# Kernel optimization log

Measured on AMD Instinct MI355X. Metric: run time of the kernel, lower is better.

The kernel has to match this reference:

```python
import jax, jax.numpy as jnp
import numpy as np
from jax import lax

B, L, DDYN, DSTAT, H = 512, 64, 16, 8, 512
N_BANK, C_CAND, K_TOP, N_PROTO = 50000, 1024, 16, 8
T_TARG, Q_QUANT = 2, 3
TEMP = 0.2


def _l2norm(x, eps=1e-12):
    # matches torch.nn.functional.normalize: x / max(||x||, eps)
    n = jnp.sqrt(jnp.sum(x * x, axis=-1, keepdims=True))
    return x / jnp.maximum(n, eps)


def setup_inputs() -> dict:
    key = jax.random.key(0)
    ks = jax.random.split(key, 24)
    s = 0.02
    inp = {
        'sequence_values': jax.random.normal(ks[0], (B, L, DDYN), jnp.float32),
        'sequence_masks': jnp.ones((B, L), jnp.float32),
        'static_values': jax.random.normal(ks[1], (B, DSTAT), jnp.float32),
        'bank_keys': jax.random.normal(ks[2], (N_BANK, H), jnp.float32),
        'bank_values': jax.random.normal(ks[3], (N_BANK, H), jnp.float32),
        'candidate_indices': jax.random.randint(ks[4], (B, C_CAND), 0, N_BANK, jnp.int64),
        # encoder params (SequenceEncoder stand-in: masked-mean + linear + relu)
        'W_seq': jax.random.normal(ks[5], (DDYN, H), jnp.float32) * s,
        'W_stat': jax.random.normal(ks[6], (DSTAT, H), jnp.float32) * s,
        'b_enc': jnp.zeros((H,), jnp.float32),
        # retrieval / prototype / fusion params
        'W_q': jax.random.normal(ks[7], (H, H), jnp.float32) * s,
        'b_q': jnp.zeros((H,), jnp.float32),
        'prototype_tokens': jax.random.normal(ks[8], (N_PROTO, H), jnp.float32) * 0.02,
        'W_tr': jax.random.normal(ks[9], (2 * H, H), jnp.float32) * s,
        'b_tr': jnp.zeros((H,), jnp.float32),
        'W_gate': jax.random.normal(ks[10], (3 * H, H), jnp.float32) * s,
        'b_gate': jnp.zeros((H,), jnp.float32),
        'W_out': jax.random.normal(ks[11], (H, H), jnp.float32) * s,
        'b_out': jnp.zeros((H,), jnp.float32),
        # per-target heads stacked: [T, H, Q] and [T, H]
        'W_quant': jax.random.normal(ks[12], (T_TARG, H, Q_QUANT), jnp.float32) * s,
        'b_quant': jnp.zeros((T_TARG, Q_QUANT), jnp.float32),
        'W_ev': jax.random.normal(ks[13], (T_TARG, H), jnp.float32) * s,
        'b_ev': jnp.zeros((T_TARG,), jnp.float32),
    }
    return inp


def reference(sequence_values, sequence_masks, static_values, bank_keys, bank_values,
              candidate_indices, W_seq, W_stat, b_enc, W_q, b_q, prototype_tokens,
              W_tr, b_tr, W_gate, b_gate, W_out, b_out, W_quant, b_quant, W_ev, b_ev):
    # --- encoder (masked mean pool + linear + relu stand-in for SequenceEncoder) ---
    m = sequence_masks[..., None]                                   # [B,L,1]
    pooled = (sequence_values * m).sum(1) / jnp.maximum(m.sum(1), 1e-6)
    local_hidden = jax.nn.relu(pooled @ W_seq + static_values @ W_stat + b_enc)  # [B,H]

    # --- normalized query ---
    query = _l2norm(local_hidden @ W_q + b_q)                       # [B,H]

    # --- donor retrieval: gather + dot + topk + softmax + weighted sum ---
    cand_keys = bank_keys[candidate_indices]                        # [B,C,H]
    sim = jnp.einsum('bch,bh->bc', cand_keys, query)                # [B,C]
    top_scores, top_pos = lax.top_k(sim, K_TOP)                     # [B,K]
    weights = jax.nn.softmax(top_scores / max(TEMP, 1e-6), axis=-1)
    sel_idx = jnp.take_along_axis(candidate_indices, top_pos, axis=1)  # [B,K]
    donor_hidden = jnp.einsum('bk,bkh->bh', weights, bank_values[sel_idx])

    # --- prototype attention ---
    protos_n = _l2norm(prototype_tokens)                            # [P,H]
    pw = jax.nn.softmax(query @ protos_n.T, axis=-1)                # [B,P]
    proto_hidden = pw @ prototype_tokens                            # [B,H]

    # --- transfer / gate / fuse (dropout is identity at eval) ---
    transfer = jax.nn.relu(jnp.concatenate([donor_hidden, proto_hidden], -1) @ W_tr + b_tr)
    gate = jax.nn.sigmoid(
        jnp.concatenate([local_hidden, donor_hidden, proto_hidden], -1) @ W_gate + b_gate)
    fused = gate * local_hidden + (1.0 - gate) * transfer
    fused = jax.nn.relu(fused @ W_out + b_out)                      # [B,H]

    # --- heads: sorted quantiles [B,T,Q] and event logits [B,T] ---
    quant = jnp.sort(jnp.einsum('bh,thq->btq', fused, W_quant) + b_quant, axis=-1)
    logit = jnp.einsum('bh,th->bt', fused, W_ev) + b_ev
    return jnp.concatenate([quant.reshape(quant.shape[0], -1), logit], axis=-1)  # [B, T*Q+T]
```

## Files before the change

kernel.cpp:

```cpp
#include <hip/hip_runtime.h>
#include <hip/hip_bf16.h>

typedef __hip_bfloat16 bf16;
typedef float f4v __attribute__((ext_vector_type(4)));
typedef float f2v __attribute__((ext_vector_type(2)));

__device__ __forceinline__ float lo16(unsigned u){ return __uint_as_float(u << 16); }
__device__ __forceinline__ float hi16(unsigned u){ return __uint_as_float(u & 0xffff0000u); }

#define Bn 512
#define Hn 512
#define Cn 1024
#define Kn 16
#define NBANK 50000
#define NIDPAD 50176

__device__ __forceinline__ int clamp_id(int id){
    return (id < 0) ? 0 : ((id >= NBANK) ? (NBANK - 1) : id);
}

#define A_OFF    0
#define B_OFF    262144
#define C_OFF    524288
#define D_OFF    786432
#define SIM_OFF  1048576
#define ELO_OFF  1048576
#define EHI_OFF  1310720
#define F_OFF    1572864
#define G_OFF2   1835008
#define WS_FLOATS 2097152

#define HIST_I   0
#define CURSOR_I NIDPAD
#define GTOT_I   (2*NIDPAD)
#define OFFS_I   (2*NIDPAD + 256)

__global__ __launch_bounds__(256) void k_enc(
    const float* __restrict__ seq, const float* __restrict__ mask, const float* __restrict__ stat,
    const float* __restrict__ W_seq, const float* __restrict__ W_stat, const float* __restrict__ b_enc,
    const int* __restrict__ cand32, float* __restrict__ ws)
{
    const int b = blockIdx.x, t = threadIdx.x;
    const int h0 = 2*t, h1 = 2*t + 1;

    {
        const int c64 = ((cand32[1] | cand32[3] | cand32[5] | cand32[7]) == 0) ? 1 : 0;
        int* hist = (int*)(ws + F_OFF) + HIST_I;
        #pragma unroll
        for (int u = 0; u < 4; u++) {
            int idx = b*Cn + u*256 + t;
            atomicAdd(&hist[clamp_id(cand32[(size_t)idx << c64])], 1);
        }
    }

    __shared__ float s_pool[16], s_stat[8];
    if (t < 16) {
        float acc = 0.f, ms = 0.f;
        for (int l = 0; l < 64; l++) {
            float m = mask[b*64 + l];
            ms  += m;
            acc += seq[(b*64 + l)*16 + t] * m;
        }
        s_pool[t] = acc / fmaxf(ms, 1e-6f);
    } else if (t < 24) {
        s_stat[t - 16] = stat[b*8 + (t - 16)];
    }
    __syncthreads();
    float a0 = b_enc[h0], a1 = b_enc[h1];
    #pragma unroll
    for (int j = 0; j < 16; j++) {
        float2 wv = *(const float2*)(W_seq + j*Hn + h0);
        a0 += s_pool[j]*wv.x; a1 += s_pool[j]*wv.y;
    }
    #pragma unroll
    for (int j = 0; j < 8; j++) {
        float2 wv = *(const float2*)(W_stat + j*Hn + h0);
        a0 += s_stat[j]*wv.x; a1 += s_stat[j]*wv.y;
    }
    float* g = ws + B_OFF + (size_t)b*Hn;
    g[h0] = fmaxf(a0, 0.f); g[h1] = fmaxf(a1, 0.f);
}

__global__ __launch_bounds__(256) void k_scan(
    const int* __restrict__ hist, int* __restrict__ offs, int* __restrict__ gtot)
{
    __shared__ int s[256]; __shared__ int sbase;
    const int t = threadIdx.x, g = blockIdx.x*256 + t;
    const int v = hist[g];
    s[t] = v; __syncthreads();
    #pragma unroll
    for (int off = 1; off < 256; off <<= 1) {
        int x = (t >= off) ? s[t - off] : 0;
        __syncthreads();
        s[t] += x;
        __syncthreads();
    }
    if (t == 255) sbase = atomicAdd(gtot, s[255]);
    __syncthreads();
    offs[g] = sbase + s[t] - v;
}

__global__ __launch_bounds__(256) void k_scatter(
    const int* __restrict__ cand32, int* __restrict__ cursor,
    const int* __restrict__ offs, unsigned* __restrict__ refs)
{
    const int i = blockIdx.x*256 + threadIdx.x;
    const int c64 = ((cand32[1] | cand32[3] | cand32[5] | cand32[7]) == 0) ? 1 : 0;
    const int id = clamp_id(cand32[(size_t)i << c64]);
    const int pos = atomicAdd(&cursor[id], 1);
    refs[offs[id] + pos] = (unsigned)i;
}

__global__ __launch_bounds__(256) void k_qgemm_p(
    const float* __restrict__ W, const float* __restrict__ bias,
    const float* __restrict__ in,
    float* __restrict__ P0, float* __restrict__ P1,
    float* __restrict__ P2, float* __restrict__ P3)
{
    const int ct = blockIdx.x, rt = blockIdx.y, kz = blockIdx.z, t = threadIdx.x;
    __shared__ float lt[64][132];
    {
        int r = t >> 2, c0 = (t & 3)*32;
        const float* src = in + (size_t)(rt*64 + r)*Hn + kz*128 + c0;
        #pragma unroll
        for (int i = 0; i < 8; i++)
            *(float4*)&lt[r][c0 + i*4] = *(const float4*)(src + i*4);
    }
    __syncthreads();
    const int col0 = ct*64 + (t & 15)*4, rbase = (t >> 4)*4;
    float acc[4][4];
    if (kz == 0) {
        float4 bv = *(const float4*)(bias + col0);
        #pragma unroll
        for (int i = 0; i < 4; i++) { acc[i][0]=bv.x; acc[i][1]=bv.y; acc[i][2]=bv.z; acc[i][3]=bv.w; }
    } else {
        #pragma unroll
        for (int i = 0; i < 4; i++) { acc[i][0]=0; acc[i][1]=0; acc[i][2]=0; acc[i][3]=0; }
    }
    const float* wp = W + (size_t)(kz*128)*Hn + col0;
    #pragma unroll 4
    for (int k = 0; k < 128; k++) {
        float4 wv = *(const float4*)(wp + (size_t)k*Hn);
        #pragma unroll
        for (int i = 0; i < 4; i++) {
            float a = lt[rbase + i][k];
            acc[i][0] += a*wv.x; acc[i][1] += a*wv.y; acc[i][2] += a*wv.z; acc[i][3] += a*wv.w;
        }
    }
    float* outp = (kz == 0) ? P0 : (kz == 1) ? P1 : (kz == 2) ? P2 : P3;
    #pragma unroll
    for (int i = 0; i < 4; i++) {
        float* op = outp + (size_t)(rt*64 + rbase + i)*Hn + col0;
        *(float4*)op = make_float4(acc[i][0], acc[i][1], acc[i][2], acc[i][3]);
    }
}

__global__ __launch_bounds__(256) void k_qnorm(float* __restrict__ ws)
{
    const int b = blockIdx.x*4 + (threadIdx.x >> 6), lane = threadIdx.x & 63;
    const size_t o = (size_t)b*Hn + lane*8;
    const float* p0 = ws + A_OFF   + o;
    const float* p1 = ws + ELO_OFF + o;
    const float* p2 = ws + EHI_OFF + o;
    const float* p3 = ws + G_OFF2  + o;
    float4 qa, qb;
    {
        float4 a0 = *(const float4*)p0, a1 = *(const float4*)p1,
               a2 = *(const float4*)p2, a3 = *(const float4*)p3;
        qa = make_float4(((a0.x+a1.x)+a2.x)+a3.x, ((a0.y+a1.y)+a2.y)+a3.y,
                         ((a0.z+a1.z)+a2.z)+a3.z, ((a0.w+a1.w)+a2.w)+a3.w);
        float4 b0 = *(const float4*)(p0+4), b1 = *(const float4*)(p1+4),
               b2 = *(const float4*)(p2+4), b3 = *(const float4*)(p3+4);
        qb = make_float4(((b0.x+b1.x)+b2.x)+b3.x, ((b0.y+b1.y)+b2.y)+b3.y,
                         ((b0.z+b1.z)+b2.z)+b3.z, ((b0.w+b1.w)+b2.w)+b3.w);
    }
    float ss = qa.x*qa.x + qa.y*qa.y + qa.z*qa.z + qa.w*qa.w
             + qb.x*qb.x + qb.y*qb.y + qb.z*qb.z + qb.w*qb.w;
    #pragma unroll
    for (int o2 = 32; o2; o2 >>= 1) ss += __shfl_xor(ss, o2);
    float inv = 1.f / fmaxf(sqrtf(ss), 1e-12f);
    qa.x *= inv; qa.y *= inv; qa.z *= inv; qa.w *= inv;
    qb.x *= inv; qb.y *= inv; qb.z *= inv; qb.w *= inv;
    float* qr = ws + A_OFF + o;
    *(float4*)qr = qa; *(float4*)(qr + 4) = qb;
}

#define DI_LOAD(R0,R1,R2,R3,A0,Bq0,A1,Bq1,A2,Bq2,A3,Bq3,BASE) do {                       \
    int j0_=(BASE), j1_=(BASE)+1, j2_=(BASE)+2, j3_=(BASE)+3;                            \
    const int m_ = n - 1;                                                                \
    const int c1_ = (j1_ < n), c2_ = (j2_ < n), c3_ = (j3_ < n);                         \
    j0_ = j0_>m_?m_:j0_; j1_ = j1_>m_?m_:j1_; j2_ = j2_>m_?m_:j2_; j3_ = j3_>m_?m_:j3_;  \
    R0 = (j0_<64)?(unsigned)__shfl((int)refv,j0_):__builtin_nontemporal_load(refs+start+j0_); \
    R1 = (j1_<64)?(unsigned)__shfl((int)refv,j1_):__builtin_nontemporal_load(refs+start+j1_); \
    R2 = (j2_<64)?(unsigned)__shfl((int)refv,j2_):__builtin_nontemporal_load(refs+start+j2_); \
    R3 = (j3_<64)?(unsigned)__shfl((int)refv,j3_):__builtin_nontemporal_load(refs+start+j3_); \
    {   const float* q0_ = qbase + (size_t)(R0>>10)*Hn + lane*8;                         \
        A0 = *(const float4*)q0_; Bq0 = *(const float4*)(q0_+4); }                       \
    if (c1_) { const float* q1_ = qbase + (size_t)(R1>>10)*Hn + lane*8;                  \
        A1 = *(const float4*)q1_; Bq1 = *(const float4*)(q1_+4); }                       \
    if (c2_) { const float* q2_ = qbase + (size_t)(R2>>10)*Hn + lane*8;                  \
        A2 = *(const float4*)q2_; Bq2 = *(const float4*)(q2_+4); }                       \
    if (c3_) { const float* q3_ = qbase + (size_t)(R3>>10)*Hn + lane*8;                  \
        A3 = *(const float4*)q3_; Bq3 = *(const float4*)(q3_+4); }                       \
} while(0)

#define DI_COMP(R0,R1,R2,R3,A0,Bq0,A1,Bq1,A2,Bq2,A3,Bq3,BASE) do {                       \
    float s0_ = ka.x*A0.x + ka.y*A0.y + ka.z*A0.z + ka.w*A0.w                            \
              + kb.x*Bq0.x + kb.y*Bq0.y + kb.z*Bq0.z + kb.w*Bq0.w;                       \
    float s1_ = ka.x*A1.x + ka.y*A1.y + ka.z*A1.z + ka.w*A1.w                            \
              + kb.x*Bq1.x + kb.y*Bq1.y + kb.z*Bq1.z + kb.w*Bq1.w;                       \
    float s2_ = ka.x*A2.x + ka.y*A2.y + ka.z*A2.z + ka.w*A2.w                            \
              + kb.x*Bq2.x + kb.y*Bq2.y + kb.z*Bq2.z + kb.w*Bq2.w;                       \
    float s3_ = ka.x*A3.x + ka.y*A3.y + ka.z*A3.z + ka.w*A3.w                            \
              + kb.x*Bq3.x + kb.y*Bq3.y + kb.z*Bq3.z + kb.w*Bq3.w;                       \
    s0_ += __shfl_xor(s0_,32); s1_ += __shfl_xor(s1_,32);                                \
    s2_ += __shfl_xor(s2_,32); s3_ += __shfl_xor(s3_,32);                                \
    s0_ += __shfl_xor(s0_,16); s1_ += __shfl_xor(s1_,16);                                \
    s2_ += __shfl_xor(s2_,16); s3_ += __shfl_xor(s3_,16);                                \
    s0_ += __shfl_xor(s0_, 8); s1_ += __shfl_xor(s1_, 8);                                \
    s2_ += __shfl_xor(s2_, 8); s3_ += __shfl_xor(s3_, 8);                                \
    int d_ = (lane >> 3) & 3;                                                            \
    float t_ = d_==0 ? s0_ : d_==1 ? s1_ : d_==2 ? s2_ : s3_;                            \
    t_ += __shfl_xor(t_, 4); t_ += __shfl_xor(t_, 2); t_ += __shfl_xor(t_, 1);           \
    if ((lane & 7) == 0 && lane < 32) {                                                  \
        int dd_ = lane >> 3;                                                             \
        if ((BASE) + dd_ < n) {                                                          \
            unsigned rs_ = dd_==0 ? R0 : dd_==1 ? R1 : dd_==2 ? R2 : R3;                 \
            simw[rs_] = t_;                                                              \
        }                                                                                \
    }                                                                                    \
} while(0)

__global__ __launch_bounds__(256) void k_dotinv(
    const float* __restrict__ bank_keys, const unsigned* __restrict__ refs,
    const int* __restrict__ offs, const int* __restrict__ cnt,
    float* __restrict__ ws)
{
    const int id = blockIdx.x*4 + (threadIdx.x >> 6);
    const int lane = threadIdx.x & 63;
    const int n = cnt[id];
    if (n <= 0) return;
    const int start = offs[id];

    const float* kp = bank_keys + (size_t)id*Hn + lane*8;
    f4v kav = __builtin_nontemporal_load((const f4v*)kp);
    f4v kbv = __builtin_nontemporal_load((const f4v*)(kp + 4));
    float4 ka = make_float4(kav.x, kav.y, kav.z, kav.w);
    float4 kb = make_float4(kbv.x, kbv.y, kbv.z, kbv.w);
    const unsigned refv = refs[start + (lane < n ? lane : n - 1)];
    const float* qbase = ws + A_OFF;
    float* simw = ws + SIM_OFF;

    unsigned Ar0,Ar1,Ar2,Ar3, Br0=0,Br1=0,Br2=0,Br3=0;
    float4 Aa0,Ab0,Aa1,Ab1,Aa2,Ab2,Aa3,Ab3;
    float4 Ba0,Bb0,Ba1,Bb1,Ba2,Bb2,Ba3,Bb3;
    Aa0=Ab0=Aa1=Ab1=Aa2=Ab2=Aa3=Ab3=make_float4(0.f,0.f,0.f,0.f);
    Ba0=Bb0=Ba1=Bb1=Ba2=Bb2=Ba3=Bb3=make_float4(0.f,0.f,0.f,0.f);

    DI_LOAD(Ar0,Ar1,Ar2,Ar3, Aa0,Ab0,Aa1,Ab1,Aa2,Ab2,Aa3,Ab3, 0);
    for (int base = 0; ; ) {
        if (base + 4 < n) DI_LOAD(Br0,Br1,Br2,Br3, Ba0,Bb0,Ba1,Bb1,Ba2,Bb2,Ba3,Bb3, base + 4);
        DI_COMP(Ar0,Ar1,Ar2,Ar3, Aa0,Ab0,Aa1,Ab1,Aa2,Ab2,Aa3,Ab3, base);
        if (base + 8 < n) DI_LOAD(Ar0,Ar1,Ar2,Ar3, Aa0,Ab0,Aa1,Ab1,Aa2,Ab2,Aa3,Ab3, base + 8);
        DI_COMP(Br0,Br1,Br2,Br3, Ba0,Bb0,Ba1,Bb1,Ba2,Bb2,Ba3,Bb3, base + 4);
        base += 8;
        if (base >= n) break;
    }
}

__global__ __launch_bounds__(256) void k_select(
    const float* __restrict__ bank_values, const int* __restrict__ cand32,
    const float* __restrict__ proto, float* __restrict__ ws)
{
    const int b = blockIdx.x, t = threadIdx.x;
    const int w = t >> 6, lane = t & 63;
    const int h0 = 2*t, h1 = 2*t + 1;
    const int c64 = ((cand32[1] | cand32[3] | cand32[5] | cand32[7]) == 0) ? 1 : 0;

    __shared__ __align__(16) float s_sim[Cn];
    __shared__ float s_bv[4]; __shared__ int s_bi[4];
    __shared__ float s_topv[Kn]; __shared__ int s_sel[Kn];
    __shared__ float s_w[Kn];
    __shared__ float s_score[8], s_pw[8];

    *(float4*)&s_sim[t*4] = *(const float4*)(ws + SIM_OFF + (size_t)b*Cn + t*4);

    const float* qr = ws + A_OFF + (size_t)b*Hn + lane*8;
    float4 qa = *(const float4*)qr, qb = *(const float4*)(qr + 4);
    float qv[8] = {qa.x, qa.y, qa.z, qa.w, qb.x, qb.y, qb.z, qb.w};
    __syncthreads();

    for (int k = 0; k < Kn; k++) {
        float best = -1e30f; int bi = 0x7fffffff;
        for (int i = t; i < Cn; i += 256) {
            float v = s_sim[i];
            if (v > best || (v == best && i < bi)) { best = v; bi = i; }
        }
        #pragma unroll
        for (int o = 32; o; o >>= 1) {
            float ov = __shfl_xor(best, o); int oi = __shfl_xor(bi, o);
            if (ov > best || (ov == best && oi < bi)) { best = ov; bi = oi; }
        }
        if (lane == 0) { s_bv[w] = best; s_bi[w] = bi; }
        __syncthreads();
        if (t == 0) {
            float bv = s_bv[0]; int bbi = s_bi[0];
            for (int x = 1; x < 4; x++)
                if (s_bv[x] > bv || (s_bv[x] == bv && s_bi[x] < bbi)) { bv = s_bv[x]; bbi = s_bi[x]; }
            if (bbi < 0 || bbi >= Cn) bbi = 0;
            s_topv[k] = bv; s_sel[k] = bbi; s_sim[bbi] = -1e30f;
        }
        __syncthreads();
    }

    if (t == 0) {
        float m = s_topv[0];
        float e[Kn], ssum = 0.f;
        for (int k = 0; k < Kn; k++) { e[k] = __expf((s_topv[k] - m) * 5.0f); ssum += e[k]; }
        float inv = 1.f / ssum;
        for (int k = 0; k < Kn; k++) s_w[k] = e[k] * inv;
    }
    for (int p = w; p < 8; p += 4) {
        const float* pp = proto + (size_t)p*Hn + lane*8;
        float4 pa = *(const float4*)pp, pb = *(const float4*)(pp + 4);
        float f[8] = {pa.x, pa.y, pa.z, pa.w, pb.x, pb.y, pb.z, pb.w};
        float dq = 0.f, sq = 0.f;
        #pragma unroll
        for (int i = 0; i < 8; i++) { dq += f[i]*qv[i]; sq += f[i]*f[i]; }
        #pragma unroll
        for (int o = 32; o; o >>= 1) { dq += __shfl_xor(dq, o); sq += __shfl_xor(sq, o); }
        if (lane == 0) s_score[p] = dq / fmaxf(sqrtf(sq), 1e-12f);
    }
    __syncthreads();
    if (t == 0) {
        float m = s_score[0];
        for (int p = 1; p < 8; p++) m = fmaxf(m, s_score[p]);
        float e[8], ssum = 0.f;
        for (int p = 0; p < 8; p++) { e[p] = __expf(s_score[p] - m); ssum += e[p]; }
        float inv = 1.f / ssum;
        for (int p = 0; p < 8; p++) s_pw[p] = e[p] * inv;
    }
    __syncthreads();

    {
        float a0 = 0.f, a1 = 0.f;
        #pragma unroll
        for (int k = 0; k < Kn; k++) {
            int id = clamp_id(cand32[(size_t)(b*Cn + s_sel[k]) << c64]);
            f2v v = __builtin_nontemporal_load((const f2v*)(bank_values + (size_t)id*Hn + h0));
            a0 += s_w[k]*v.x; a1 += s_w[k]*v.y;
        }
        float* gd = ws + C_OFF + (size_t)b*Hn;
        gd[h0] = a0; gd[h1] = a1;
    }
    {
        float a0 = 0.f, a1 = 0.f;
        #pragma unroll
        for (int p = 0; p < 8; p++) {
            float2 v = *(const float2*)(proto + (size_t)p*Hn + h0);
            a0 += s_pw[p]*v.x; a1 += s_pw[p]*v.y;
        }
        float* gp = ws + D_OFF + (size_t)b*Hn;
        gp[h0] = a0; gp[h1] = a1;
    }
}

__global__ __launch_bounds__(256) void k_gatetr_p(
    const float* __restrict__ W_tr, const float* __restrict__ b_tr,
    const float* __restrict__ W_gate, const float* __restrict__ b_gate,
    float* __restrict__ ws)
{
    const int ct = blockIdx.x, rt = blockIdx.y, z = blockIdx.z, t = threadIdx.x;
    const int isGate = (z < 3);
    const int sl = isGate ? z : (z - 3);
    const float* W = isGate ? (W_gate + (size_t)(z*512)*Hn) : (W_tr + (size_t)(sl*512)*Hn);
    const float* slab = ws + B_OFF + (size_t)(isGate ? z : (sl + 1))*262144;
    float* outp = isGate
        ? ((z == 0) ? ws + A_OFF : (z == 1) ? ws + ELO_OFF : ws + EHI_OFF)
        : ((sl == 0) ? ws + F_OFF : ws + G_OFF2);

    __shared__ float lt[32][260];
    const int col0 = ct*128 + (t & 31)*4, rbase = (t >> 5)*4;
    float acc[4][4];
    if (z == 0 || z == 3) {
        const float* bias = isGate ? b_gate : b_tr;
        float4 bv = *(const float4*)(bias + col0);
        #pragma unroll
        for (int i = 0; i < 4; i++) { acc[i][0]=bv.x; acc[i][1]=bv.y; acc[i][2]=bv.z; acc[i][3]=bv.w; }
    } else {
        #pragma unroll
        for (int i = 0; i < 4; i++) { acc[i][0]=0; acc[i][1]=0; acc[i][2]=0; acc[i][3]=0; }
    }

    #pragma unroll
    for (int h = 0; h < 2; h++) {
        if (h) __syncthreads();
        {
            int r = t >> 3, c0 = (t & 7)*32;
            const float* src = slab + (size_t)(rt*32 + r)*Hn + h*256 + c0;
            #pragma unroll
            for (int i = 0; i < 8; i++)
                *(float4*)&lt[r][c0 + i*4] = *(const float4*)(src + i*4);
        }
        __syncthreads();
        const float* wp = W + (size_t)(h*256)*Hn + col0;
        #pragma unroll 4
        for (int k = 0; k < 256; k++) {
            float4 wv = *(const float4*)(wp + (size_t)k*Hn);
            #pragma unroll
            for (int i = 0; i < 4; i++) {
                float a = lt[rbase + i][k];
                acc[i][0] += a*wv.x; acc[i][1] += a*wv.y; acc[i][2] += a*wv.z; acc[i][3] += a*wv.w;
            }
        }
    }
    #pragma unroll
    for (int i = 0; i < 4; i++) {
        float* op = outp + (size_t)(rt*32 + rbase + i)*Hn + col0;
        *(float4*)op = make_float4(acc[i][0], acc[i][1], acc[i][2], acc[i][3]);
    }
}

__global__ __launch_bounds__(256) void k_f1ew(float* __restrict__ ws)
{
    const int i4 = blockIdx.x*256 + threadIdx.x;
    const size_t off = (size_t)(i4 >> 7)*Hn + (i4 & 127)*4;
    float4 lc = *(const float4*)(ws + B_OFF + off);
    float4 g0 = *(const float4*)(ws + A_OFF + off);
    float4 g1 = *(const float4*)(ws + ELO_OFF + off);
    float4 g2 = *(const float4*)(ws + EHI_OFF + off);
    float4 t0 = *(const float4*)(ws + F_OFF + off);
    float4 t1 = *(const float4*)(ws + G_OFF2 + off);
    float4 ga = make_float4((g0.x+g1.x)+g2.x, (g0.y+g1.y)+g2.y,
                            (g0.z+g1.z)+g2.z, (g0.w+g1.w)+g2.w);
    float4 tr = make_float4(t0.x+t1.x, t0.y+t1.y, t0.z+t1.z, t0.w+t1.w);
    float4 r;
    float s;
    s = 1.f/(1.f + __expf(-ga.x)); r.x = s*lc.x + (1.f-s)*fmaxf(tr.x, 0.f);
    s = 1.f/(1.f + __expf(-ga.y)); r.y = s*lc.y + (1.f-s)*fmaxf(tr.y, 0.f);
    s = 1.f/(1.f + __expf(-ga.z)); r.z = s*lc.z + (1.f-s)*fmaxf(tr.z, 0.f);
    s = 1.f/(1.f + __expf(-ga.w)); r.w = s*lc.w + (1.f-s)*fmaxf(tr.w, 0.f);
    *(float4*)(ws + A_OFF + off) = r;
}

__global__ __launch_bounds__(64) void k_heads(
    const float* __restrict__ W_quant, const float* __restrict__ b_quant,
    const float* __restrict__ W_ev, const float* __restrict__ b_ev,
    const float* __restrict__ ws_ro, float* __restrict__ out)
{
    const int b = blockIdx.x, lane = threadIdx.x;
    const size_t o = (size_t)b*Hn + lane*8;
    const float* p0 = ws_ro + ELO_OFF + o;
    const float* p1 = ws_ro + EHI_OFF + o;
    const float* p2 = ws_ro + F_OFF + o;
    const float* p3 = ws_ro + G_OFF2 + o;
    float4 a0 = *(const float4*)p0, a1 = *(const float4*)p1,
           a2 = *(const float4*)p2, a3 = *(const float4*)p3;
    float4 b0 = *(const float4*)(p0+4), b1 = *(const float4*)(p1+4),
           b2 = *(const float4*)(p2+4), b3 = *(const float4*)(p3+4);
    float fv[8] = {
        fmaxf(((a0.x+a1.x)+a2.x)+a3.x, 0.f), fmaxf(((a0.y+a1.y)+a2.y)+a3.y, 0.f),
        fmaxf(((a0.z+a1.z)+a2.z)+a3.z, 0.f), fmaxf(((a0.w+a1.w)+a2.w)+a3.w, 0.f),
        fmaxf(((b0.x+b1.x)+b2.x)+b3.x, 0.f), fmaxf(((b0.y+b1.y)+b2.y)+b3.y, 0.f),
        fmaxf(((b0.z+b1.z)+b2.z)+b3.z, 0.f), fmaxf(((b0.w+b1.w)+b2.w)+b3.w, 0.f)};
    float acc[8];
    #pragma unroll
    for (int q = 0; q < 8; q++) acc[q] = 0.f;
    #pragma unroll
    for (int i = 0; i < 8; i++) {
        int h = lane*8 + i;
        float fh = fv[i];
        acc[0] += fh*W_quant[(0*Hn + h)*3 + 0];
        acc[1] += fh*W_quant[(0*Hn + h)*3 + 1];
        acc[2] += fh*W_quant[(0*Hn + h)*3 + 2];
        acc[3] += fh*W_quant[(1*Hn + h)*3 + 0];
        acc[4] += fh*W_quant[(1*Hn + h)*3 + 1];
        acc[5] += fh*W_quant[(1*Hn + h)*3 + 2];
        acc[6] += fh*W_ev[0*Hn + h];
        acc[7] += fh*W_ev[1*Hn + h];
    }
    #pragma unroll
    for (int q = 0; q < 8; q++) {
        #pragma unroll
        for (int s = 32; s; s >>= 1) acc[q] += __shfl_xor(acc[q], s);
    }
    if (lane == 0) {
        float qv[6];
        for (int q = 0; q < 6; q++) qv[q] = acc[q] + b_quant[q];
        #pragma unroll
        for (int tt = 0; tt < 2; tt++) {
            float a = qv[tt*3], bb = qv[tt*3+1], c = qv[tt*3+2];
            float mn = fminf(a, fminf(bb, c)), mx = fmaxf(a, fmaxf(bb, c));
            float md = a + bb + c - mn - mx;
            qv[tt*3] = mn; qv[tt*3+1] = md; qv[tt*3+2] = mx;
        }
        for (int q = 0; q < 6; q++) out[b*8 + q] = qv[q];
        out[b*8 + 6] = acc[6] + b_ev[0];
        out[b*8 + 7] = acc[7] + b_ev[1];
    }
}

__device__ __forceinline__ float lds_f(const void* p, int i, int f32){
    return f32 ? ((const float*)p)[i] : __bfloat162float(((const bf16*)p)[i]);
}
__device__ __forceinline__ float2 ldpair(const void* p, int elt, int f32){
    if (f32) return ((const float2*)p)[elt >> 1];
    unsigned u = ((const unsigned*)p)[elt >> 1];
    return make_float2(lo16(u), hi16(u));
}
__device__ __forceinline__ void ld8(const void* p, int elt, int f32, float* v){
    if (f32){
        const float4* q = (const float4*)((const float*)p + elt);
        float4 a = q[0], b = q[1];
        v[0]=a.x; v[1]=a.y; v[2]=a.z; v[3]=a.w; v[4]=b.x; v[5]=b.y; v[6]=b.z; v[7]=b.w;
    } else {
        uint4 u = *(const uint4*)((const bf16*)p + elt);
        v[0]=lo16(u.x); v[1]=hi16(u.x); v[2]=lo16(u.y); v[3]=hi16(u.y);
        v[4]=lo16(u.z); v[5]=hi16(u.z); v[6]=lo16(u.w); v[7]=hi16(u.w);
    }
}
__device__ __forceinline__ void st_out(void* o, int i, int f32, float v){
    if (f32) ((float*)o)[i] = v; else ((bf16*)o)[i] = __float2bfloat16(v);
}

__global__ __launch_bounds__(256) void k_fused(
    const void* __restrict__ seq, const void* __restrict__ mask, const void* __restrict__ stat,
    const void* __restrict__ bank_keys, const void* __restrict__ bank_values,
    const int* __restrict__ cand32,
    const void* __restrict__ W_seq, const void* __restrict__ W_stat, const void* __restrict__ b_enc,
    const void* __restrict__ W_q, const void* __restrict__ b_q,
    const void* __restrict__ proto,
    const void* __restrict__ W_tr, const void* __restrict__ b_tr,
    const void* __restrict__ W_gate, const void* __restrict__ b_gate,
    const void* __restrict__ W_out, const void* __restrict__ b_out,
    const void* __restrict__ W_quant, const void* __restrict__ b_quant,
    const void* __restrict__ W_ev, const void* __restrict__ b_ev,
    void* __restrict__ out)
{
    const int b = blockIdx.x, t = threadIdx.x;
    const int w = t >> 6, lane = t & 63;
    const int h0 = 2*t, h1 = 2*t + 1;
    const int f32 = (((const unsigned short*)mask)[0] == 0) ? 1 : 0;
    const int c64 = ((cand32[1] | cand32[3] | cand32[5] | cand32[7]) == 0) ? 1 : 0;

    __shared__ __align__(16) float s_pool[16];
    __shared__ __align__(16) float s_stat[8];
    __shared__ __align__(16) float g[1536];
    __shared__ __align__(16) float s_q[Hn];
    __shared__ __align__(16) float s_sim[Cn];
    __shared__ __align__(16) float f1[Hn];
    __shared__ __align__(16) float f2[Hn];
    __shared__ float s_part[4], s_ss;
    __shared__ float s_bv[4]; __shared__ int s_bi[4];
    __shared__ float s_topv[Kn]; __shared__ int s_sel[Kn];
    __shared__ float s_w[Kn];
    __shared__ float s_score[8], s_pw[8];
    __shared__ float s_head[8][4];

    if (t < 16) {
        float acc = 0.f, ms = 0.f;
        for (int l = 0; l < 64; l++) {
            float m = lds_f(mask, b*64 + l, f32);
            ms  += m;
            acc += lds_f(seq, (b*64 + l)*16 + t, f32) * m;
        }
        s_pool[t] = acc / fmaxf(ms, 1e-6f);
    } else if (t < 24) {
        s_stat[t - 16] = lds_f(stat, b*8 + (t - 16), f32);
    }
    __syncthreads();
    {
        float a0 = lds_f(b_enc, h0, f32), a1 = lds_f(b_enc, h1, f32);
        #pragma unroll
        for (int j = 0; j < 16; j++) {
            float2 wv = ldpair(W_seq, j*Hn + h0, f32);
            a0 += s_pool[j]*wv.x; a1 += s_pool[j]*wv.y;
        }
        #pragma unroll
        for (int j = 0; j < 8; j++) {
            float2 wv = ldpair(W_stat, j*Hn + h0, f32);
            a0 += s_stat[j]*wv.x; a1 += s_stat[j]*wv.y;
        }
        a0 = fmaxf(a0, 0.f); a1 = fmaxf(a1, 0.f);
        g[h0] = a0; g[h1] = a1;
    }
    __syncthreads();
    {
        float q0 = lds_f(b_q, h0, f32), q1 = lds_f(b_q, h1, f32);
        #pragma unroll 4
        for (int j = 0; j < Hn; j++) {
            float lj = g[j];
            float2 wv = ldpair(W_q, j*Hn + h0, f32);
            q0 += lj*wv.x; q1 += lj*wv.y;
        }
        float ss = q0*q0 + q1*q1;
        #pragma unroll
        for (int o = 32; o; o >>= 1) ss += __shfl_xor(ss, o);
        if (lane == 0) s_part[w] = ss;
        __syncthreads();
        if (t == 0) s_ss = s_part[0] + s_part[1] + s_part[2] + s_part[3];
        __syncthreads();
        float inv = 1.f / fmaxf(sqrtf(s_ss), 1e-12f);
        s_q[h0] = q0*inv; s_q[h1] = q1*inv;
    }
    __syncthreads();
    float qv[8];
    #pragma unroll
    for (int i = 0; i < 8; i++) qv[i] = s_q[lane*8 + i];

    for (int c0 = w*256; c0 < w*256 + 256; c0 += 4) {
        float kf[4][8];
        #pragma unroll
        for (int u = 0; u < 4; u++) {
            int id = clamp_id(cand32[(size_t)(b*Cn + c0 + u) << c64]);
            ld8(bank_keys, id*Hn + lane*8, f32, kf[u]);
        }
        #pragma unroll
        for (int u = 0; u < 4; u++) {
            float s = 0.f;
            #pragma unroll
            for (int i = 0; i < 8; i++) s += kf[u][i]*qv[i];
            #pragma unroll
            for (int o = 32; o; o >>= 1) s += __shfl_xor(s, o);
            if (lane == 0) s_sim[c0 + u] = s;
        }
    }
    __syncthreads();
    for (int k = 0; k < Kn; k++) {
        float best = -1e30f; int bi = 0x7fffffff;
        for (int i = t; i < Cn; i += 256) {
            float v = s_sim[i];
            if (v > best || (v == best && i < bi)) { best = v; bi = i; }
        }
        #pragma unroll
        for (int o = 32; o; o >>= 1) {
            float ov = __shfl_xor(best, o); int oi = __shfl_xor(bi, o);
            if (ov > best || (ov == best && oi < bi)) { best = ov; bi = oi; }
        }
        if (lane == 0) { s_bv[w] = best; s_bi[w] = bi; }
        __syncthreads();
        if (t == 0) {
            float bv = s_bv[0]; int bbi = s_bi[0];
            for (int x = 1; x < 4; x++)
                if (s_bv[x] > bv || (s_bv[x] == bv && s_bi[x] < bbi)) { bv = s_bv[x]; bbi = s_bi[x]; }
            if (bbi < 0 || bbi >= Cn) bbi = 0;
            s_topv[k] = bv; s_sel[k] = bbi; s_sim[bbi] = -1e30f;
        }
        __syncthreads();
    }
    if (t == 0) {
        float m = s_topv[0];
        float e[Kn], ssum = 0.f;
        for (int k = 0; k < Kn; k++) { e[k] = __expf((s_topv[k] - m) * 5.0f); ssum += e[k]; }
        float inv = 1.f / ssum;
        for (int k = 0; k < Kn; k++) s_w[k] = e[k] * inv;
    }
    __syncthreads();
    {
        float a0 = 0.f, a1 = 0.f;
        #pragma unroll
        for (int k = 0; k < Kn; k++) {
            int id = clamp_id(cand32[(size_t)(b*Cn + s_sel[k]) << c64]);
            float2 v = ldpair(bank_values, id*Hn + h0, f32);
            a0 += s_w[k]*v.x; a1 += s_w[k]*v.y;
        }
        g[512 + h0] = a0; g[512 + h1] = a1;
    }
    for (int p = w; p < 8; p += 4) {
        float f[8];
        ld8(proto, p*Hn + lane*8, f32, f);
        float dq = 0.f, sq = 0.f;
        #pragma unroll
        for (int i = 0; i < 8; i++) { dq += f[i]*qv[i]; sq += f[i]*f[i]; }
        #pragma unroll
        for (int o = 32; o; o >>= 1) { dq += __shfl_xor(dq, o); sq += __shfl_xor(sq, o); }
        if (lane == 0) s_score[p] = dq / fmaxf(sqrtf(sq), 1e-12f);
    }
    __syncthreads();
    if (t == 0) {
        float m = s_score[0];
        for (int p = 1; p < 8; p++) m = fmaxf(m, s_score[p]);
        float e[8], ssum = 0.f;
        for (int p = 0; p < 8; p++) { e[p] = __expf(s_score[p] - m); ssum += e[p]; }
        float inv = 1.f / ssum;
        for (int p = 0; p < 8; p++) s_pw[p] = e[p] * inv;
    }
    __syncthreads();
    {
        float a0 = 0.f, a1 = 0.f;
        #pragma unroll
        for (int p = 0; p < 8; p++) {
            float2 v = ldpair(proto, p*Hn + h0, f32);
            a0 += s_pw[p]*v.x; a1 += s_pw[p]*v.y;
        }
        g[1024 + h0] = a0; g[1024 + h1] = a1;
    }
    __syncthreads();
    float tr0 = lds_f(b_tr, h0, f32), tr1 = lds_f(b_tr, h1, f32);
    #pragma unroll 4
    for (int j = 0; j < 1024; j++) {
        float gj = g[512 + j];
        float2 wv = ldpair(W_tr, j*Hn + h0, f32);
        tr0 += gj*wv.x; tr1 += gj*wv.y;
    }
    tr0 = fmaxf(tr0, 0.f); tr1 = fmaxf(tr1, 0.f);
    float gt0 = lds_f(b_gate, h0, f32), gt1 = lds_f(b_gate, h1, f32);
    #pragma unroll 4
    for (int j = 0; j < 1536; j++) {
        float gj = g[j];
        float2 wv = ldpair(W_gate, j*Hn + h0, f32);
        gt0 += gj*wv.x; gt1 += gj*wv.y;
    }
    gt0 = 1.f/(1.f + __expf(-gt0)); gt1 = 1.f/(1.f + __expf(-gt1));
    f1[h0] = gt0*g[h0] + (1.f - gt0)*tr0;
    f1[h1] = gt1*g[h1] + (1.f - gt1)*tr1;
    __syncthreads();
    {
        float o0 = lds_f(b_out, h0, f32), o1 = lds_f(b_out, h1, f32);
        #pragma unroll 4
        for (int j = 0; j < Hn; j++) {
            float fj = f1[j];
            float2 wv = ldpair(W_out, j*Hn + h0, f32);
            o0 += fj*wv.x; o1 += fj*wv.y;
        }
        o0 = fmaxf(o0, 0.f); o1 = fmaxf(o1, 0.f);
        f2[h0] = o0; f2[h1] = o1;
    }
    __syncthreads();
    {
        float acc[8];
        #pragma unroll
        for (int o = 0; o < 8; o++) acc[o] = 0.f;
        for (int h = t; h < Hn; h += 256) {
            float fh = f2[h];
            acc[0] += fh*lds_f(W_quant, (0*Hn + h)*3 + 0, f32);
            acc[1] += fh*lds_f(W_quant, (0*Hn + h)*3 + 1, f32);
            acc[2] += fh*lds_f(W_quant, (0*Hn + h)*3 + 2, f32);
            acc[3] += fh*lds_f(W_quant, (1*Hn + h)*3 + 0, f32);
            acc[4] += fh*lds_f(W_quant, (1*Hn + h)*3 + 1, f32);
            acc[5] += fh*lds_f(W_quant, (1*Hn + h)*3 + 2, f32);
            acc[6] += fh*lds_f(W_ev, 0*Hn + h, f32);
            acc[7] += fh*lds_f(W_ev, 1*Hn + h, f32);
        }
        #pragma unroll
        for (int o = 0; o < 8; o++) {
            float v = acc[o];
            #pragma unroll
            for (int s = 32; s; s >>= 1) v += __shfl_xor(v, s);
            if (lane == 0) s_head[o][w] = v;
        }
        __syncthreads();
        if (t == 0) {
            float q[6];
            for (int o = 0; o < 6; o++)
                q[o] = s_head[o][0] + s_head[o][1] + s_head[o][2] + s_head[o][3] + lds_f(b_quant, o, f32);
            #pragma unroll
            for (int tt = 0; tt < 2; tt++) {
                float a = q[tt*3], bb = q[tt*3+1], c = q[tt*3+2];
                float mn = fminf(a, fminf(bb, c)), mx = fmaxf(a, fmaxf(bb, c));
                float md = a + bb + c - mn - mx;
                q[tt*3] = mn; q[tt*3+1] = md; q[tt*3+2] = mx;
            }
            for (int o = 0; o < 6; o++) st_out(out, b*8 + o, f32, q[o]);
            float l0 = s_head[6][0] + s_head[6][1] + s_head[6][2] + s_head[6][3] + lds_f(b_ev, 0, f32);
            float l1 = s_head[7][0] + s_head[7][1] + s_head[7][2] + s_head[7][3] + lds_f(b_ev, 1, f32);
            st_out(out, b*8 + 6, f32, l0);
            st_out(out, b*8 + 7, f32, l1);
        }
    }
}

extern "C" void kernel_launch(void* const* d_in, const int* in_sizes, int n_in,
                              void* d_out, int out_size, void* d_ws, size_t ws_size,
                              hipStream_t stream) {
    static const int expect[22] = {
        512*64*16, 512*64, 512*8, 50000*512, 50000*512, 512*1024,
        16*512, 8*512, 512, 512*512, 512, 8*512,
        1024*512, 512, 1536*512, 512, 512*512, 512,
        2*512*3, 2*3, 2*512, 2
    };
    if (n_in != 22 || out_size != 512*8) return;
    for (int i = 0; i < 22; i++) if (in_sizes[i] != expect[i]) return;

    if (ws_size < (size_t)WS_FLOATS * 4) {
        k_fused<<<Bn, 256, 0, stream>>>(
            d_in[0], d_in[1], d_in[2], d_in[3], d_in[4], (const int*)d_in[5],
            d_in[6], d_in[7], d_in[8], d_in[9], d_in[10], d_in[11],
            d_in[12], d_in[13], d_in[14], d_in[15], d_in[16], d_in[17],
            d_in[18], d_in[19], d_in[20], d_in[21], d_out);
        return;
    }

    float* ws = (float*)d_ws;
    int* iws = (int*)(ws + F_OFF);
    int* hist   = iws + HIST_I;
    int* cursor = iws + CURSOR_I;
    int* gtot   = iws + GTOT_I;
    int* offs   = iws + OFFS_I;
    unsigned* refs = (unsigned*)(ws + C_OFF);

    hipMemsetAsync(iws, 0, (size_t)(2*NIDPAD + 256)*4, stream);

    k_enc<<<Bn, 256, 0, stream>>>((const float*)d_in[0], (const float*)d_in[1],
                                  (const float*)d_in[2], (const float*)d_in[6],
                                  (const float*)d_in[7], (const float*)d_in[8],
                                  (const int*)d_in[5], ws);
    k_scan<<<NIDPAD/256, 256, 0, stream>>>(hist, offs, gtot);
    k_scatter<<<(Bn*Cn)/256, 256, 0, stream>>>((const int*)d_in[5], cursor, offs, refs);
    k_qgemm_p<<<dim3(8, 8, 4), 256, 0, stream>>>(
        (const float*)d_in[9], (const float*)d_in[10], ws + B_OFF,
        ws + A_OFF, ws + ELO_OFF, ws + EHI_OFF, ws + G_OFF2);
    k_qnorm<<<Bn/4, 256, 0, stream>>>(ws);
    k_dotinv<<<NBANK/4, 256, 0, stream>>>((const float*)d_in[3], refs, offs, hist, ws);
    k_select<<<Bn, 256, 0, stream>>>((const float*)d_in[4], (const int*)d_in[5],
                                     (const float*)d_in[11], ws);
    k_gatetr_p<<<dim3(4, 16, 5), 256, 0, stream>>>(
        (const float*)d_in[12], (const float*)d_in[13],
        (const float*)d_in[14], (const float*)d_in[15], ws);
    k_f1ew<<<256, 256, 0, stream>>>(ws);
    k_qgemm_p<<<dim3(8, 8, 4), 256, 0, stream>>>(
        (const float*)d_in[16], (const float*)d_in[17], ws + A_OFF,
        ws + ELO_OFF, ws + EHI_OFF, ws + F_OFF, ws + G_OFF2);
    k_heads<<<Bn, 64, 0, stream>>>((const float*)d_in[18], (const float*)d_in[19],
                                   (const float*)d_in[20], (const float*)d_in[21],
                                   ws, (float*)d_out);
}
```

Before: 500.4 us.

## Fuse encoder, query GEMM and L2 norm into one kernel per four rows

The encoder kernel now handles four batch rows per block, keeps the encoded hidden in shared memory, and computes the W_q projection and L2 normalisation in place. This removes the split-K query GEMM launch, the qnorm launch and the partial-sum round trips through workspace. The cursor reset moves into the scan kernel, so the memset covers less. In exchange only 128 blocks run the 512x512 GEMM with a plain FMA loop, which may leave much of the GPU idle on that part.

Result: slower. 538.5 us (+7.6%).

```diff
diff --git a/kernel.cpp b/kernel.cpp
--- a/kernel.cpp
+++ b/kernel.cpp
@@ -31,62 +31,116 @@
 #define WS_FLOATS 2097152
 
 #define HIST_I   0
-#define CURSOR_I NIDPAD
-#define GTOT_I   (2*NIDPAD)
+#define GTOT_I   NIDPAD
+#define CURSOR_I (NIDPAD + 256)
 #define OFFS_I   (2*NIDPAD + 256)
 
-__global__ __launch_bounds__(256) void k_enc(
+__global__ __launch_bounds__(256) void k_encq(
     const float* __restrict__ seq, const float* __restrict__ mask, const float* __restrict__ stat,
     const float* __restrict__ W_seq, const float* __restrict__ W_stat, const float* __restrict__ b_enc,
+    const float* __restrict__ W_q, const float* __restrict__ b_q,
     const int* __restrict__ cand32, float* __restrict__ ws)
 {
-    const int b = blockIdx.x, t = threadIdx.x;
+    const int b0 = blockIdx.x*4, t = threadIdx.x;
+    const int w = t >> 6, lane = t & 63;
     const int h0 = 2*t, h1 = 2*t + 1;
-
-    {
-        const int c64 = ((cand32[1] | cand32[3] | cand32[5] | cand32[7]) == 0) ? 1 : 0;
+    const int c64 = ((cand32[1] | cand32[3] | cand32[5] | cand32[7]) == 0) ? 1 : 0;
+
+    {
         int* hist = (int*)(ws + F_OFF) + HIST_I;
         #pragma unroll
-        for (int u = 0; u < 4; u++) {
-            int idx = b*Cn + u*256 + t;
+        for (int u = 0; u < 16; u++) {
+            int idx = b0*Cn + u*256 + t;
             atomicAdd(&hist[clamp_id(cand32[(size_t)idx << c64])], 1);
         }
     }
 
-    __shared__ float s_pool[16], s_stat[8];
-    if (t < 16) {
+    __shared__ float s_pool[4][16], s_stat[4][8];
+    __shared__ __align__(16) float g[4][Hn];
+    __shared__ float s_part[4][4], s_ss[4];
+
+    if (lane < 16) {
+        const int b = b0 + w;
         float acc = 0.f, ms = 0.f;
         for (int l = 0; l < 64; l++) {
             float m = mask[b*64 + l];
             ms  += m;
-            acc += seq[(b*64 + l)*16 + t] * m;
-        }
-        s_pool[t] = acc / fmaxf(ms, 1e-6f);
-    } else if (t < 24) {
-        s_stat[t - 16] = stat[b*8 + (t - 16)];
-    }
-    __syncthreads();
-    float a0 = b_enc[h0], a1 = b_enc[h1];
-    #pragma unroll
-    for (int j = 0; j < 16; j++) {
-        float2 wv = *(const float2*)(W_seq + j*Hn + h0);
-        a0 += s_pool[j]*wv.x; a1 += s_pool[j]*wv.y;
-    }
-    #pragma unroll
-    for (int j = 0; j < 8; j++) {
-        float2 wv = *(const float2*)(W_stat + j*Hn + h0);
-        a0 += s_stat[j]*wv.x; a1 += s_stat[j]*wv.y;
-    }
-    float* g = ws + B_OFF + (size_t)b*Hn;
-    g[h0] = fmaxf(a0, 0.f); g[h1] = fmaxf(a1, 0.f);
+            acc += seq[(b*64 + l)*16 + lane] * m;
+        }
+        s_pool[w][lane] = acc / fmaxf(ms, 1e-6f);
+    } else if (lane < 24) {
+        s_stat[w][lane - 16] = stat[(b0 + w)*8 + (lane - 16)];
+    }
+    __syncthreads();
+
+    {
+        float a0[4], a1[4];
+        float be0 = b_enc[h0], be1 = b_enc[h1];
+        #pragma unroll
+        for (int r = 0; r < 4; r++) { a0[r] = be0; a1[r] = be1; }
+        #pragma unroll
+        for (int j = 0; j < 16; j++) {
+            float2 wv = *(const float2*)(W_seq + j*Hn + h0);
+            #pragma unroll
+            for (int r = 0; r < 4; r++) { a0[r] += s_pool[r][j]*wv.x; a1[r] += s_pool[r][j]*wv.y; }
+        }
+        #pragma unroll
+        for (int j = 0; j < 8; j++) {
+            float2 wv = *(const float2*)(W_stat + j*Hn + h0);
+            #pragma unroll
+            for (int r = 0; r < 4; r++) { a0[r] += s_stat[r][j]*wv.x; a1[r] += s_stat[r][j]*wv.y; }
+        }
+        #pragma unroll
+        for (int r = 0; r < 4; r++) {
+            float v0 = fmaxf(a0[r], 0.f), v1 = fmaxf(a1[r], 0.f);
+            g[r][h0] = v0; g[r][h1] = v1;
+            float* gl = ws + B_OFF + (size_t)(b0 + r)*Hn;
+            gl[h0] = v0; gl[h1] = v1;
+        }
+    }
+    __syncthreads();
+
+    float q0[4], q1[4];
+    {
+        float bq0 = b_q[h0], bq1 = b_q[h1];
+        #pragma unroll
+        for (int r = 0; r < 4; r++) { q0[r] = bq0; q1[r] = bq1; }
+        #pragma unroll 4
+        for (int j = 0; j < Hn; j++) {
+            float2 wv = *(const float2*)(W_q + j*Hn + h0);
+            #pragma unroll
+            for (int r = 0; r < 4; r++) {
+                float gj = g[r][j];
+                q0[r] += gj*wv.x; q1[r] += gj*wv.y;
+            }
+        }
+    }
+    #pragma unroll
+    for (int r = 0; r < 4; r++) {
+        float ss = q0[r]*q0[r] + q1[r]*q1[r];
+        #pragma unroll
+        for (int o = 32; o; o >>= 1) ss += __shfl_xor(ss, o);
+        if (lane == 0) s_part[r][w] = ss;
+    }
+    __syncthreads();
+    if (t < 4) s_ss[t] = s_part[t][0] + s_part[t][1] + s_part[t][2] + s_part[t][3];
+    __syncthreads();
+    #pragma unroll
+    for (int r = 0; r < 4; r++) {
+        float inv = 1.f / fmaxf(sqrtf(s_ss[r]), 1e-12f);
+        float* qr = ws + A_OFF + (size_t)(b0 + r)*Hn;
+        qr[h0] = q0[r]*inv; qr[h1] = q1[r]*inv;
+    }
 }
 
 __global__ __launch_bounds__(256) void k_scan(
-    const int* __restrict__ hist, int* __restrict__ offs, int* __restrict__ gtot)
+    const int* __restrict__ hist, int* __restrict__ offs, int* __restrict__ gtot,
+    int* __restrict__ cursor)
 {
     __shared__ int s[256]; __shared__ int sbase;
     const int t = threadIdx.x, g = blockIdx.x*256 + t;
     const int v = hist[g];
+    cursor[g] = 0;
     s[t] = v; __syncthreads();
     #pragma unroll
     for (int off = 1; off < 256; off <<= 1) {
@@ -153,36 +207,6 @@
         float* op = outp + (size_t)(rt*64 + rbase + i)*Hn + col0;
         *(float4*)op = make_float4(acc[i][0], acc[i][1], acc[i][2], acc[i][3]);
     }
-}
-
-__global__ __launch_bounds__(256) void k_qnorm(float* __restrict__ ws)
-{
-    const int b = blockIdx.x*4 + (threadIdx.x >> 6), lane = threadIdx.x & 63;
-    const size_t o = (size_t)b*Hn + lane*8;
-    const float* p0 = ws + A_OFF   + o;
-    const float* p1 = ws + ELO_OFF + o;
-    const float* p2 = ws + EHI_OFF + o;
-    const float* p3 = ws + G_OFF2  + o;
-    float4 qa, qb;
-    {
-        float4 a0 = *(const float4*)p0, a1 = *(const float4*)p1,
-               a2 = *(const float4*)p2, a3 = *(const float4*)p3;
-        qa = make_float4(((a0.x+a1.x)+a2.x)+a3.x, ((a0.y+a1.y)+a2.y)+a3.y,
-                         ((a0.z+a1.z)+a2.z)+a3.z, ((a0.w+a1.w)+a2.w)+a3.w);
-        float4 b0 = *(const float4*)(p0+4), b1 = *(const float4*)(p1+4),
-               b2 = *(const float4*)(p2+4), b3 = *(const float4*)(p3+4);
-        qb = make_float4(((b0.x+b1.x)+b2.x)+b3.x, ((b0.y+b1.y)+b2.y)+b3.y,
-                         ((b0.z+b1.z)+b2.z)+b3.z, ((b0.w+b1.w)+b2.w)+b3.w);
-    }
-    float ss = qa.x*qa.x + qa.y*qa.y + qa.z*qa.z + qa.w*qa.w
-             + qb.x*qb.x + qb.y*qb.y + qb.z*qb.z + qb.w*qb.w;
-    #pragma unroll
-    for (int o2 = 32; o2; o2 >>= 1) ss += __shfl_xor(ss, o2);
-    float inv = 1.f / fmaxf(sqrtf(ss), 1e-12f);
-    qa.x *= inv; qa.y *= inv; qa.z *= inv; qa.w *= inv;
-    qb.x *= inv; qb.y *= inv; qb.z *= inv; qb.w *= inv;
-    float* qr = ws + A_OFF + o;
-    *(float4*)qr = qa; *(float4*)(qr + 4) = qb;
 }
 
 #define DI_LOAD(R0,R1,R2,R3,A0,Bq0,A1,Bq1,A2,Bq2,A3,Bq3,BASE) do {                       \
@@ -794,23 +818,20 @@
     float* ws = (float*)d_ws;
     int* iws = (int*)(ws + F_OFF);
     int* hist   = iws + HIST_I;
+    int* gtot   = iws + GTOT_I;
     int* cursor = iws + CURSOR_I;
-    int* gtot   = iws + GTOT_I;
     int* offs   = iws + OFFS_I;
     unsigned* refs = (unsigned*)(ws + C_OFF);
 
-    hipMemsetAsync(iws, 0, (size_t)(2*NIDPAD + 256)*4, stream);
-
-    k_enc<<<Bn, 256, 0, stream>>>((const float*)d_in[0], (const float*)d_in[1],
-                                  (const float*)d_in[2], (const float*)d_in[6],
-                                  (const float*)d_in[7], (const float*)d_in[8],
-                                  (const int*)d_in[5], ws);
-    k_scan<<<NIDPAD/256, 256, 0, stream>>>(hist, offs, gtot);
+    hipMemsetAsync(iws, 0, (size_t)(NIDPAD + 256)*4, stream);
+
+    k_encq<<<Bn/4, 256, 0, stream>>>(
+        (const float*)d_in[0], (const float*)d_in[1], (const float*)d_in[2],
+        (const float*)d_in[6], (const float*)d_in[7], (const float*)d_in[8],
+        (const float*)d_in[9], (const float*)d_in[10],
+        (const int*)d_in[5], ws);
+    k_scan<<<NIDPAD/256, 256, 0, stream>>>(hist, offs, gtot, cursor);
     k_scatter<<<(Bn*Cn)/256, 256, 0, stream>>>((const int*)d_in[5], cursor, offs, refs);
-    k_qgemm_p<<<dim3(8, 8, 4), 256, 0, stream>>>(
-        (const float*)d_in[9], (const float*)d_in[10], ws + B_OFF,
-        ws + A_OFF, ws + ELO_OFF, ws + EHI_OFF, ws + G_OFF2);
-    k_qnorm<<<Bn/4, 256, 0, stream>>>(ws);
     k_dotinv<<<NBANK/4, 256, 0, stream>>>((const float*)d_in[3], refs, offs, hist, ws);
     k_select<<<Bn, 256, 0, stream>>>((const float*)d_in[4], (const int*)d_in[5],
                                      (const float*)d_in[11], ws);
```
